# Kernel tuning notes

Hardware: AMD Instinct MI355X
Metric: run time of the kernel (lower is better)

Reference implementation:

```python
import jax, jax.numpy as jnp
import numpy as np

B, T, C, H, HD = 2, 2048, 2048, 16, 128
RD = HD // 2          # rope_dim = 64 (32 complex pairs)
KVR, QR = 512, 1024   # kv_lora_rank, q_lora_rank


def setup_inputs() -> dict:
    key = jax.random.key(0)
    ks = jax.random.split(key, 10)
    s = 0.02
    x = jax.random.normal(ks[0], (B, T, C), jnp.float32)
    w_dq  = jax.random.normal(ks[1], (C, QR),     jnp.float32) * s
    w_uq  = jax.random.normal(ks[2], (QR, H * HD), jnp.float32) * s
    w_dkv = jax.random.normal(ks[3], (C, KVR),    jnp.float32) * s
    w_uk  = jax.random.normal(ks[4], (KVR, H * HD), jnp.float32) * s
    w_uv  = jax.random.normal(ks[5], (KVR, H * HD), jnp.float32) * s
    w_qr  = jax.random.normal(ks[6], (QR, H * RD), jnp.float32) * s
    w_kr  = jax.random.normal(ks[7], (C, H * RD), jnp.float32) * s
    w_o   = jax.random.normal(ks[8], (H * HD, C), jnp.float32) * s
    # rotary frequencies for the rope_dim part (rope_dim//2 = 32 complex freqs)
    inv_freq = 1.0 / (10000.0 ** (jnp.arange(0, RD, 2, dtype=jnp.float32) / RD))
    ang = jnp.arange(T, dtype=jnp.float32)[:, None] * inv_freq[None, :]  # (T, 32)
    return {"x": x, "w_dq": w_dq, "w_uq": w_uq, "w_dkv": w_dkv, "w_uk": w_uk,
            "w_uv": w_uv, "w_qr": w_qr, "w_kr": w_kr, "w_o": w_o,
            "freqs_cos": jnp.cos(ang), "freqs_sin": jnp.sin(ang)}


def _apply_rope(t, cos, sin):
    # t: (B, T, H, rd); cos/sin: (T, rd//2). Complex rotation on adjacent pairs.
    tr, ti = t[..., 0::2], t[..., 1::2]
    c = cos[None, :, None, :]
    s = sin[None, :, None, :]
    out_r = tr * c - ti * s
    out_i = tr * s + ti * c
    return jnp.stack([out_r, out_i], axis=-1).reshape(t.shape)


def reference(x, w_dq, w_uq, w_dkv, w_uk, w_uv, w_qr, w_kr, w_o, freqs_cos, freqs_sin):
    b, t, _ = x.shape
    # low-rank KV path
    c_kv = x @ w_dkv                                   # (B,T,KVR)
    k_c = (c_kv @ w_uk).reshape(b, t, H, HD)
    v   = (c_kv @ w_uv).reshape(b, t, H, HD)
    # low-rank Q path
    c_q = x @ w_dq                                     # (B,T,QR)
    q_c = (c_q @ w_uq).reshape(b, t, H, HD)
    # decoupled rope parts
    q_r = (c_q @ w_qr).reshape(b, t, H, RD)
    k_r = (x @ w_kr).reshape(b, t, H, RD)
    q_r = _apply_rope(q_r, freqs_cos, freqs_sin)
    k_r = _apply_rope(k_r, freqs_cos, freqs_sin)
    # concat content + rope -> head dim D = HD + RD
    q = jnp.concatenate([q_c, q_r], axis=-1).transpose(0, 2, 1, 3)  # (B,H,T,D)
    k = jnp.concatenate([k_c, k_r], axis=-1).transpose(0, 2, 1, 3)
    v = v.transpose(0, 2, 1, 3)                                     # (B,H,T,HD)
    d = q.shape[-1]
    scores = jnp.einsum('bhqd,bhkd->bhqk', q, k) / jnp.sqrt(jnp.float32(d))
    causal = jnp.tril(jnp.ones((t, t), dtype=bool))
    scores = jnp.where(causal[None, None], scores, jnp.float32(-1e30))
    att = jax.nn.softmax(scores, axis=-1)
    out = jnp.einsum('bhqk,bhkd->bhqd', att, v)        # (B,H,T,HD)
    out = out.transpose(0, 2, 1, 3).reshape(b, t, H * HD)
    return out @ w_o
```

## Files before the change

kernel.cpp:

```cpp
#include <hip/hip_runtime.h>

typedef unsigned short ushort_t;
typedef __attribute__((ext_vector_type(8))) short bs8;
typedef __attribute__((ext_vector_type(4))) float f32x4;
typedef __attribute__((ext_vector_type(4))) unsigned short u16x4;

#define DEV __device__ __forceinline__

DEV unsigned short f2bf(float f){
  unsigned u = __float_as_uint(f);
  u += 0x7fffu + ((u >> 16) & 1u);
  return (unsigned short)(u >> 16);
}
DEV float bf2f(unsigned short h){ return __uint_as_float(((unsigned)h) << 16); }

DEV unsigned cvt_pk_bf16(float lo, float hi){
  unsigned r;
  asm volatile("v_cvt_pk_bf16_f32 %0, %1, %2" : "=v"(r) : "v"(lo), "v"(hi));
  return r;
}

DEV void gl2lds16(const void* g, void* l){
  __builtin_amdgcn_global_load_lds((const __attribute__((address_space(1))) void*)g,
                                   (__attribute__((address_space(3))) void*)l, 16, 0, 0);
}

DEV void st_out(ushort_t* C, size_t i, float v){ C[i] = f2bf(v); }
DEV void st_out(float*    C, size_t i, float v){ C[i] = v; }

__global__ __launch_bounds__(256) void cast_x(const float* __restrict__ in,
                                              ushort_t* __restrict__ outb){
  size_t i = ((size_t)blockIdx.x * 256 + threadIdx.x) * 4;
  float4 v = *(const float4*)(in + i);
  u16x4 o;
  o[0] = f2bf(v.x); o[1] = f2bf(v.y); o[2] = f2bf(v.z); o[3] = f2bf(v.w);
  *(u16x4*)(outb + i) = o;
}

__global__ __launch_bounds__(256) void transpose_cast(const float* __restrict__ in,
                                                      ushort_t* __restrict__ out,
                                                      int K, int N){
  __shared__ float tile[32][33];
  int k0 = blockIdx.y * 32, n0 = blockIdx.x * 32;
  int tx = threadIdx.x, ty = threadIdx.y;
  for (int r = ty; r < 32; r += 8)
    tile[r][tx] = in[(size_t)(k0 + r) * N + n0 + tx];
  __syncthreads();
  for (int r = ty; r < 32; r += 8)
    out[(size_t)(n0 + r) * K + k0 + tx] = f2bf(tile[tx][r]);
}

__global__ __launch_bounds__(256) void transpose_v(const ushort_t* __restrict__ v, int ldv,
                                                   ushort_t* __restrict__ vT){
  __shared__ ushort_t tile[32][33];
  int bh = blockIdx.z; int b = bh >> 4, h = bh & 15;
  int t0 = blockIdx.x * 32, d0 = blockIdx.y * 32;
  int tx = threadIdx.x, ty = threadIdx.y;
  for (int r = ty; r < 32; r += 8)
    tile[r][tx] = v[((size_t)(b * 2048 + t0 + r)) * ldv + h * 128 + d0 + tx];
  __syncthreads();
  for (int r = ty; r < 32; r += 8)
    vT[((size_t)bh * 128 + d0 + r) * 2048 + t0 + tx] = tile[tx][r];
}

template<int EPI, typename OT>
__global__ __launch_bounds__(512, 2) void gemm256(const ushort_t* __restrict__ A, int lda,
                                                  const ushort_t* __restrict__ BT,
                                                  OT* __restrict__ C,
                                                  int M, int N, int K,
                                                  ushort_t* __restrict__ aux,
                                                  const float* __restrict__ fcp,
                                                  const float* __restrict__ fsp){
  __shared__ __align__(16) ushort_t lds[65536];
  const int tid = threadIdx.x, lane = tid & 63, wid = tid >> 6;
  const int l15 = lane & 15, lhi = lane >> 4;
  const int wr = wid >> 2, wc = wid & 3;

  const int nbx = M >> 8;
  const int nwg = gridDim.x;
  const int orig = blockIdx.x;
  const int wg = (orig & 7) * (nwg >> 3) + (orig >> 3);
  const int m0 = (wg % nbx) << 8;
  const int n0 = (wg / nbx) << 8;

  const int trow = tid >> 3;
  const int tcsrc = (tid & 7) ^ (trow & 7);
  const ushort_t* gA[2][2];
  const ushort_t* gB[2][2];
#pragma unroll
  for (int h = 0; h < 2; ++h)
#pragma unroll
    for (int i = 0; i < 2; ++i){
      gA[h][i] = A  + (size_t)(m0 + h * 128 + i * 64 + trow) * lda + tcsrc * 8;
      gB[h][i] = BT + (size_t)(n0 + h * 128 + i * 64 + trow) * K   + tcsrc * 8;
    }

  auto STAGE_A = [&](int buf, int h, int kt){
    gl2lds16(gA[h][0] + (size_t)kt * 64, lds + buf * 32768 + h * 8192 + tid * 8);
    gl2lds16(gA[h][1] + (size_t)kt * 64, lds + buf * 32768 + h * 8192 + 4096 + tid * 8);
  };
  auto STAGE_B = [&](int buf, int h, int kt){
    gl2lds16(gB[h][0] + (size_t)kt * 64, lds + buf * 32768 + 16384 + h * 8192 + tid * 8);
    gl2lds16(gB[h][1] + (size_t)kt * 64, lds + buf * 32768 + 16384 + h * 8192 + 4096 + tid * 8);
  };

  const int ck0 = ((lhi) ^ (l15 & 7)) << 3;
  const int ck1 = ((4 + lhi) ^ (l15 & 7)) << 3;

  f32x4 acc[8][4] = {};
  bs8 aF[4][2], bLo[2][2], bHi[2][2];

  auto RDA = [&](int buf, int mq){
#pragma unroll
    for (int m = 0; m < 4; ++m){
      const ushort_t* r = lds + buf * 32768 + wr * 8192 + ((mq + m) * 16 + l15) * 64;
      aF[m][0] = *(const bs8*)(r + ck0);
      aF[m][1] = *(const bs8*)(r + ck1);
    }
  };
  auto RDB = [&](int buf, int nq, bs8 (&br)[2][2]){
#pragma unroll
    for (int n = 0; n < 2; ++n){
      const ushort_t* r = lds + buf * 32768 + 16384 + (wc >> 1) * 8192 +
                          ((wc & 1) * 64 + (nq + n) * 16 + l15) * 64;
      br[n][0] = *(const bs8*)(r + ck0);
      br[n][1] = *(const bs8*)(r + ck1);
    }
  };
  auto MMA = [&](int mq, int nq, bs8 (&br)[2][2]){
    __builtin_amdgcn_s_setprio(1);
#pragma unroll
    for (int m = 0; m < 4; ++m)
#pragma unroll
      for (int n = 0; n < 2; ++n){
        acc[mq + m][nq + n] = __builtin_amdgcn_mfma_f32_16x16x32_bf16(aF[m][0], br[n][0], acc[mq + m][nq + n], 0, 0, 0);
        acc[mq + m][nq + n] = __builtin_amdgcn_mfma_f32_16x16x32_bf16(aF[m][1], br[n][1], acc[mq + m][nq + n], 0, 0, 0);
      }
    __builtin_amdgcn_s_setprio(0);
  };

#define BAR() __builtin_amdgcn_s_barrier()
#define LGK() asm volatile("s_waitcnt lgkmcnt(0)" ::: "memory")
#define VMC4() asm volatile("s_waitcnt vmcnt(4)" ::: "memory")

  const int nkt = K >> 6;
  const int nIter = K >> 7;

  STAGE_A(0, 0, 0); STAGE_A(0, 1, 0); STAGE_B(0, 0, 0); STAGE_B(0, 1, 0);
  STAGE_B(1, 0, 1); STAGE_B(1, 1, 1);
  VMC4();
  BAR();

  for (int it = 0; it < nIter; ++it){
    const int kt1 = 2 * it + 1;
    int kt2 = 2 * it + 2; if (kt2 > nkt - 1) kt2 = nkt - 1;
    int kt3 = 2 * it + 3; if (kt3 > nkt - 1) kt3 = nkt - 1;
    RDA(0, 0); RDB(0, 0, bLo);
    STAGE_A(1, 0, kt1);
    BAR(); LGK(); MMA(0, 0, bLo); BAR();
    RDB(0, 2, bHi);
    STAGE_A(1, 1, kt1);
    BAR(); LGK(); MMA(0, 2, bHi); BAR();
    RDA(0, 4);
    STAGE_B(0, 0, kt2);
    BAR(); LGK(); MMA(4, 0, bLo); BAR();
    STAGE_B(0, 1, kt2);
    BAR(); LGK(); MMA(4, 2, bHi);
    VMC4(); BAR();
    RDA(1, 0); RDB(1, 0, bLo);
    STAGE_A(0, 0, kt2);
    BAR(); LGK(); MMA(0, 0, bLo); BAR();
    RDB(1, 2, bHi);
    STAGE_A(0, 1, kt2);
    BAR(); LGK(); MMA(0, 2, bHi); BAR();
    RDA(1, 4);
    STAGE_B(1, 0, kt3);
    BAR(); LGK(); MMA(4, 0, bLo); BAR();
    STAGE_B(1, 1, kt3);
    BAR(); LGK(); MMA(4, 2, bHi);
    VMC4(); BAR();
  }
#undef BAR
#undef LGK
#undef VMC4

  const float SC = (EPI == 2) ? (0.07216878364870323f * 1.4426950408889634f) : 1.0f;
  const int RBASE = (EPI == 1) ? 1536 : 2048;
#pragma unroll
  for (int m = 0; m < 8; ++m){
    const int r = m0 + wr * 128 + m * 16 + lhi * 4;
#pragma unroll
    for (int n = 0; n < 4; ++n){
      const int c = n0 + wc * 64 + n * 16 + l15;
      if (EPI == 0){
#pragma unroll
        for (int j = 0; j < 4; ++j)
          st_out(C, (size_t)(r + j) * N + c, acc[m][n][j]);
      } else if ((EPI == 1 && c < 1536)){
#pragma unroll
        for (int j = 0; j < 4; ++j)
          C[(size_t)(r + j) * 1536 + c] = (OT)f2bf(acc[m][n][j]);
      } else if (EPI == 2 && c < 2048){
        int hh = c >> 7, d = c & 127;
#pragma unroll
        for (int j = 0; j < 4; ++j){
          int rr = r + j, bb = rr >> 11, tt = rr & 2047;
          aux[((size_t)(bb * 16 + hh) * 2048 + tt) * 192 + d] = f2bf(acc[m][n][j] * SC);
        }
      } else if (EPI == 3 && c < 2048){
        int hh = c >> 7, d = c & 127;
#pragma unroll
        for (int j = 0; j < 4; ++j){
          int rr = r + j, bb = rr >> 11, tt = rr & 2047;
          aux[((size_t)(bb * 16 + hh) * 2048 + tt) * 192 + d] = f2bf(acc[m][n][j]);
        }
      } else if (EPI == 3){
#pragma unroll
        for (int j = 0; j < 4; ++j)
          C[(size_t)(r + j) * 2048 + (c - 2048)] = (OT)f2bf(acc[m][n][j]);
      } else {
        int cr = c - RBASE;
        int hh = cr >> 6, dr = cr & 63, ii = dr >> 1;
#pragma unroll
        for (int j = 0; j < 4; ++j){
          int rr = r + j, bb = rr >> 11, tt = rr & 2047;
          float v = acc[m][n][j] * SC;
          float pv = __shfl_xor(v, 1);
          float co = fcp[tt * 32 + ii], si = fsp[tt * 32 + ii];
          float o = (l15 & 1) ? fmaf(pv, si, v * co) : fmaf(-pv, si, v * co);
          aux[((size_t)(bb * 16 + hh) * 2048 + tt) * 192 + 128 + dr] = f2bf(o);
        }
      }
    }
  }
}

__global__ __launch_bounds__(512, 1) void attn_kernel(const ushort_t* __restrict__ Qa,
                                                      const ushort_t* __restrict__ Ka,
                                                      const ushort_t* __restrict__ VT,
                                                      ushort_t* __restrict__ O){
  __shared__ __align__(16) ushort_t lds[40960];
  const int tid = threadIdx.x, lane = tid & 63, wid = tid >> 6;
  const int bh = blockIdx.x, p = blockIdx.y;
  const int b = bh >> 4, h = bh & 15;
  const int qb0 = 15 - p, qb1 = p;
  const int nkt0 = 2 * qb0 + 2;
  const int NT = 34;
  const int l15 = lane & 15, lhi = lane >> 4;

  const ushort_t* Kbh = Ka + (size_t)bh * 2048 * 192;
  const ushort_t* Vbh = VT + (size_t)bh * 128 * 2048;

  const ushort_t* ksrc[3];
#pragma unroll
  for (int i = 0; i < 3; ++i){
    int c = i * 512 + tid;
    int row = c / 24, col = c % 24;
    int hk = (row & 3) | (((row >> 3) & 1) << 2);
    ksrc[i] = Kbh + (size_t)row * 192 + (col ^ hk) * 8;
  }
  const ushort_t* vsrc[2];
#pragma unroll
  for (int i = 0; i < 2; ++i){
    int c = i * 512 + tid;
    int d = c >> 3, col = c & 7;
    vsrc[i] = Vbh + (size_t)d * 2048 + (col ^ (d & 7)) * 8;
  }

  auto STAGE = [&](int ft, int buf){
    int kt = (ft < nkt0) ? ft : ft - nkt0;
#pragma unroll
    for (int i = 0; i < 3; ++i)
      gl2lds16(ksrc[i] + (size_t)kt * 12288, lds + buf * 12288 + (i * 512 + tid) * 8);
#pragma unroll
    for (int i = 0; i < 2; ++i)
      gl2lds16(vsrc[i] + kt * 64, lds + 24576 + buf * 8192 + (i * 512 + tid) * 8);
  };

  bs8 qf[6];
  auto LOADQ = [&](int qb){
    const size_t qrow = ((size_t)bh * 2048 + qb * 128 + wid * 16 + l15) * 192;
#pragma unroll
    for (int kc = 0; kc < 6; ++kc)
      qf[kc] = *(const bs8*)(Qa + qrow + kc * 32 + lhi * 8);
  };

  f32x4 acc[8] = {};
  float mrow = -1e30f, lrow = 0.f;

  auto EPI = [&](int qb){
    float rl = 1.0f / lrow;
    int t = qb * 128 + wid * 16 + l15;
#pragma unroll
    for (int f = 0; f < 8; ++f){
      u16x4 o;
#pragma unroll
      for (int j = 0; j < 4; ++j) o[j] = f2bf(acc[f][j] * rl);
      *(u16x4*)(O + ((size_t)b * 2048 + t) * 2048 + h * 128 + f * 16 + lhi * 4) = o;
    }
  };

  const int hkr = (l15 & 3) | (((l15 >> 2) & 1) << 2);

#define BARR() __builtin_amdgcn_s_barrier()
#define LGK0() asm volatile("s_waitcnt lgkmcnt(0)" ::: "memory")
#define VMC(n) asm volatile("s_waitcnt vmcnt(" #n ")" ::: "memory")

  LOADQ(qb0);
  STAGE(0, 0);
  STAGE(1, 1);
  VMC(5);
  BARR();

  for (int ft = 0; ft < NT; ++ft){
    if (ft == nkt0){
      EPI(qb0);
#pragma unroll
      for (int f = 0; f < 8; ++f) acc[f] = (f32x4){0.f, 0.f, 0.f, 0.f};
      mrow = -1e30f; lrow = 0.f;
      LOADQ(qb1);
    }
    const int seg = (ft >= nkt0) ? 1 : 0;
    const int kt = seg ? ft - nkt0 : ft;
    const int qb = seg ? qb1 : qb0;
    const int qm0 = qb << 7;
    const int mylast = 2 * qb + (wid >> 2);
    const int cur = ft & 1;
    const ushort_t* Kb = lds + cur * 12288;
    const ushort_t* Vb = lds + 24576 + cur * 8192;

    if (kt <= mylast){
      f32x4 s[4] = {};
      __builtin_amdgcn_s_setprio(1);
#pragma unroll
      for (int kc = 0; kc < 6; ++kc){
        bs8 kf4[4];
#pragma unroll
        for (int m = 0; m < 4; ++m){
          int row = ((m >> 1) << 5) + ((l15 >> 2) << 3) + ((m & 1) << 2) + (l15 & 3);
          kf4[m] = *(const bs8*)(Kb + row * 192 + (((kc * 4 + lhi) ^ hkr) << 3));
        }
#pragma unroll
        for (int m = 0; m < 4; ++m)
          s[m] = __builtin_amdgcn_mfma_f32_16x16x32_bf16(kf4[m], qf[kc], s[m], 0, 0, 0);
      }
      __builtin_amdgcn_s_setprio(0);

      const bool noMask = (kt * 64 + 63) <= (qm0 + wid * 16);
      const int qi = qm0 + wid * 16 + l15;
      float rmax = -3e38f;
#pragma unroll
      for (int m = 0; m < 4; ++m)
#pragma unroll
        for (int j = 0; j < 4; ++j){
          float sv = s[m][j];
          if (!noMask){
            int ki = kt * 64 + ((m >> 1) << 5) + (lhi << 3) + ((m & 1) << 2) + j;
            if (ki > qi) sv = -3e38f;
          }
          s[m][j] = sv;
          rmax = fmaxf(rmax, sv);
        }
      rmax = fmaxf(rmax, __shfl_xor(rmax, 16));
      rmax = fmaxf(rmax, __shfl_xor(rmax, 32));
      if (!__all(rmax <= mrow + 8.f)){
        float mnew = fmaxf(mrow, rmax);
        float osc = exp2f(mrow - mnew);
        lrow *= osc;
#pragma unroll
        for (int f = 0; f < 8; ++f) acc[f] *= osc;
        mrow = mnew;
      }
      float rsum = 0.f;
#pragma unroll
      for (int m = 0; m < 4; ++m)
#pragma unroll
        for (int j = 0; j < 4; ++j){
          float pv = exp2f(s[m][j] - mrow);
          s[m][j] = pv;
          rsum += pv;
        }
      rsum += __shfl_xor(rsum, 16);
      rsum += __shfl_xor(rsum, 32);
      lrow += rsum;

      bs8 pb[2];
#pragma unroll
      for (int kc2 = 0; kc2 < 2; ++kc2){
        union { bs8 v; unsigned u[4]; } pu;
#pragma unroll
        for (int half = 0; half < 2; ++half){
          const f32x4& sv = s[2 * kc2 + half];
          pu.u[2 * half]     = cvt_pk_bf16(sv[0], sv[1]);
          pu.u[2 * half + 1] = cvt_pk_bf16(sv[2], sv[3]);
        }
        pb[kc2] = pu.v;
      }

      __builtin_amdgcn_s_setprio(1);
#pragma unroll
      for (int kc2 = 0; kc2 < 2; ++kc2)
#pragma unroll
        for (int f = 0; f < 8; ++f){
          bs8 vf = *(const bs8*)(Vb + (f * 16 + l15) * 64 + (((kc2 * 4 + lhi) ^ (l15 & 7)) << 3));
          acc[f] = __builtin_amdgcn_mfma_f32_16x16x32_bf16(vf, pb[kc2], acc[f], 0, 0, 0);
        }
      __builtin_amdgcn_s_setprio(0);
    }

    LGK0();
    BARR();
    if (ft + 2 < NT){
      STAGE(ft + 2, cur);
      VMC(5);
    } else {
      VMC(0);
    }
    BARR();
  }
#undef BARR
#undef LGK0
#undef VMC

  EPI(qb1);
}

extern "C" void kernel_launch(void* const* d_in, const int* in_sizes, int n_in,
                              void* d_out, int out_size, void* d_ws, size_t ws_size,
                              hipStream_t stream){
  constexpr int Bc = 2, Tc = 2048, Cc = 2048, Hc = 16, HDc = 128, RDc = 64, KVRc = 512, QRc = 1024;
  constexpr int Mx = Bc * Tc;
  const float* x     = (const float*)d_in[0];
  const float* w_dq  = (const float*)d_in[1];
  const float* w_uq  = (const float*)d_in[2];
  const float* w_dkv = (const float*)d_in[3];
  const float* w_uk  = (const float*)d_in[4];
  const float* w_uv  = (const float*)d_in[5];
  const float* w_qr  = (const float*)d_in[6];
  const float* w_kr  = (const float*)d_in[7];
  const float* w_o   = (const float*)d_in[8];
  const float* fc    = (const float*)d_in[9];
  const float* fs    = (const float*)d_in[10];
  float* out = (float*)d_out;

  char* ws = (char*)d_ws;
  size_t off = 0;
  auto alloc = [&](size_t elems) -> ushort_t* {
    ushort_t* p = (ushort_t*)(ws + off);
    off += ((elems * 2) + 255) & ~(size_t)255;
    return p;
  };
  ushort_t* xb    = alloc((size_t)Mx * Cc);
  ushort_t* wdqT  = alloc((size_t)QRc * Cc);
  ushort_t* wdkvT = alloc((size_t)KVRc * Cc);
  ushort_t* wkrT  = alloc((size_t)(Hc * RDc) * Cc);
  ushort_t* wuqT  = alloc((size_t)(Hc * HDc) * QRc);
  ushort_t* wqrT  = alloc((size_t)(Hc * RDc) * QRc);
  ushort_t* wukT  = alloc((size_t)(Hc * HDc) * KVRc);
  ushort_t* wuvT  = alloc((size_t)(Hc * HDc) * KVRc);
  ushort_t* woT   = alloc((size_t)Cc * (Hc * HDc));
  ushort_t* comb1 = alloc((size_t)Mx * 1536);
  ushort_t* vb    = alloc((size_t)Mx * 2048);
  ushort_t* Qa    = alloc((size_t)Bc * Hc * Tc * 192);
  ushort_t* Ka    = alloc((size_t)Bc * Hc * Tc * 192);
  ushort_t* vT    = alloc((size_t)Bc * Hc * HDc * Tc);
  ushort_t* O     = xb;

  cast_x<<<dim3(((size_t)Mx * Cc) / 1024), 256, 0, stream>>>(x, xb);

  transpose_cast<<<dim3(QRc / 32, Cc / 32), dim3(32, 8), 0, stream>>>(w_dq, wdqT, Cc, QRc);
  transpose_cast<<<dim3(KVRc / 32, Cc / 32), dim3(32, 8), 0, stream>>>(w_dkv, wdkvT, Cc, KVRc);
  transpose_cast<<<dim3((Hc * RDc) / 32, Cc / 32), dim3(32, 8), 0, stream>>>(w_kr, wkrT, Cc, Hc * RDc);
  transpose_cast<<<dim3((Hc * HDc) / 32, QRc / 32), dim3(32, 8), 0, stream>>>(w_uq, wuqT, QRc, Hc * HDc);
  transpose_cast<<<dim3((Hc * RDc) / 32, QRc / 32), dim3(32, 8), 0, stream>>>(w_qr, wqrT, QRc, Hc * RDc);
  transpose_cast<<<dim3((Hc * HDc) / 32, KVRc / 32), dim3(32, 8), 0, stream>>>(w_uk, wukT, KVRc, Hc * HDc);
  transpose_cast<<<dim3((Hc * HDc) / 32, KVRc / 32), dim3(32, 8), 0, stream>>>(w_uv, wuvT, KVRc, Hc * HDc);
  transpose_cast<<<dim3(Cc / 32, (Hc * HDc) / 32), dim3(32, 8), 0, stream>>>(w_o, woT, Hc * HDc, Cc);

  gemm256<1, ushort_t><<<dim3((Mx / 256) * (2560 / 256)), 512, 0, stream>>>(
      xb, Cc, wdqT, comb1, Mx, 2560, Cc, Ka, fc, fs);
  gemm256<2, ushort_t><<<dim3((Mx / 256) * (3072 / 256)), 512, 0, stream>>>(
      comb1, 1536, wuqT, Qa , Mx, 3072, QRc, Qa, fc, fs);
  gemm256<3, ushort_t><<<dim3((Mx / 256) * (4096 / 256)), 512, 0, stream>>>(
      comb1 + QRc, 1536, wukT, vb, Mx, 4096, KVRc, Ka, fc, fs);

  transpose_v<<<dim3(Tc / 32, HDc / 32, Bc * Hc), dim3(32, 8), 0, stream>>>(vb, 2048, vT);

  attn_kernel<<<dim3(Bc * Hc, 8), 512, 0, stream>>>(Qa, Ka, vT, O);

  gemm256<0, float><<<dim3((Mx / 256) * (Cc / 256)), 512, 0, stream>>>(
      O, Hc * HDc, woT, out, Mx, Cc, Hc * HDc, nullptr, nullptr, nullptr);
}
```

Before: 317.3 us.

## Batch weight casts, merge up-projection GEMMs, split attention KV tiles across wave halves

Replaces eight transpose-cast launches with one flat-grid kernel, and fuses the Q and K/V up-projection GEMMs into a single 448-block launch so they share one wave of work. In attention, each wave now handles 32 query rows and the two wave halves process alternating KV tiles, then merge partial softmax states through extra LDS at the epilogue. This aims to cut launch overhead, tail effects and causal load imbalance, at the cost of more LDS, more registers for the attention kernel and an extra merge step.

```diff
diff --git a/kernel.cpp b/kernel.cpp
--- a/kernel.cpp
+++ b/kernel.cpp
@@ -37,17 +37,34 @@
   *(u16x4*)(outb + i) = o;
 }
 
-__global__ __launch_bounds__(256) void transpose_cast(const float* __restrict__ in,
-                                                      ushort_t* __restrict__ out,
-                                                      int K, int N){
+__global__ __launch_bounds__(256) void tcast_all(
+    const float* __restrict__ s0, const float* __restrict__ s1,
+    const float* __restrict__ s2, const float* __restrict__ s3,
+    const float* __restrict__ s4, const float* __restrict__ s5,
+    const float* __restrict__ s6, const float* __restrict__ s7,
+    ushort_t* __restrict__ d0, ushort_t* __restrict__ d1,
+    ushort_t* __restrict__ d2, ushort_t* __restrict__ d3,
+    ushort_t* __restrict__ d4, ushort_t* __restrict__ d5,
+    ushort_t* __restrict__ d6, ushort_t* __restrict__ d7){
   __shared__ float tile[32][33];
-  int k0 = blockIdx.y * 32, n0 = blockIdx.x * 32;
-  int tx = threadIdx.x, ty = threadIdx.y;
+  const int bid = blockIdx.x;
+  const float* src; ushort_t* dst; int K, N, loc;
+  if      (bid <  2048){ src=s0; dst=d0; K=2048; N=1024; loc=bid; }
+  else if (bid <  3072){ src=s1; dst=d1; K=2048; N=512;  loc=bid-2048; }
+  else if (bid <  5120){ src=s2; dst=d2; K=2048; N=1024; loc=bid-3072; }
+  else if (bid <  7168){ src=s3; dst=d3; K=1024; N=2048; loc=bid-5120; }
+  else if (bid <  8192){ src=s4; dst=d4; K=1024; N=1024; loc=bid-7168; }
+  else if (bid <  9216){ src=s5; dst=d5; K=512;  N=2048; loc=bid-8192; }
+  else if (bid < 10240){ src=s6; dst=d6; K=512;  N=2048; loc=bid-9216; }
+  else                 { src=s7; dst=d7; K=2048; N=2048; loc=bid-10240; }
+  const int nx = N >> 5;
+  const int n0 = (loc % nx) << 5, k0 = (loc / nx) << 5;
+  const int tx = threadIdx.x & 31, ty = threadIdx.x >> 5;
   for (int r = ty; r < 32; r += 8)
-    tile[r][tx] = in[(size_t)(k0 + r) * N + n0 + tx];
+    tile[r][tx] = src[(size_t)(k0 + r) * N + n0 + tx];
   __syncthreads();
   for (int r = ty; r < 32; r += 8)
-    out[(size_t)(n0 + r) * K + k0 + tx] = f2bf(tile[tx][r]);
+    dst[(size_t)(n0 + r) * K + k0 + tx] = f2bf(tile[tx][r]);
 }
 
 __global__ __launch_bounds__(256) void transpose_v(const ushort_t* __restrict__ v, int ldv,
@@ -63,25 +80,12 @@
     vT[((size_t)bh * 128 + d0 + r) * 2048 + t0 + tx] = tile[tx][r];
 }
 
-template<int EPI, typename OT>
-__global__ __launch_bounds__(512, 2) void gemm256(const ushort_t* __restrict__ A, int lda,
-                                                  const ushort_t* __restrict__ BT,
-                                                  OT* __restrict__ C,
-                                                  int M, int N, int K,
-                                                  ushort_t* __restrict__ aux,
-                                                  const float* __restrict__ fcp,
-                                                  const float* __restrict__ fsp){
-  __shared__ __align__(16) ushort_t lds[65536];
+DEV void gemm_core(const ushort_t* __restrict__ A, int lda,
+                   const ushort_t* __restrict__ BT, int K,
+                   int m0, int n0, ushort_t* lds, f32x4 (&acc)[8][4]){
   const int tid = threadIdx.x, lane = tid & 63, wid = tid >> 6;
   const int l15 = lane & 15, lhi = lane >> 4;
   const int wr = wid >> 2, wc = wid & 3;
-
-  const int nbx = M >> 8;
-  const int nwg = gridDim.x;
-  const int orig = blockIdx.x;
-  const int wg = (orig & 7) * (nwg >> 3) + (orig >> 3);
-  const int m0 = (wg % nbx) << 8;
-  const int n0 = (wg / nbx) << 8;
 
   const int trow = tid >> 3;
   const int tcsrc = (tid & 7) ^ (trow & 7);
@@ -107,7 +111,6 @@
   const int ck0 = ((lhi) ^ (l15 & 7)) << 3;
   const int ck1 = ((4 + lhi) ^ (l15 & 7)) << 3;
 
-  f32x4 acc[8][4] = {};
   bs8 aF[4][2], bLo[2][2], bHi[2][2];
 
   auto RDA = [&](int buf, int mq){
@@ -183,7 +186,15 @@
 #undef BAR
 #undef LGK
 #undef VMC4
-
+}
+
+template<int EPI, typename OT>
+DEV void gemm_epi(f32x4 (&acc)[8][4], OT* __restrict__ C, int N, int m0, int n0,
+                  ushort_t* __restrict__ aux,
+                  const float* __restrict__ fcp, const float* __restrict__ fsp){
+  const int tid = threadIdx.x, lane = tid & 63, wid = tid >> 6;
+  const int l15 = lane & 15, lhi = lane >> 4;
+  const int wr = wid >> 2, wc = wid & 3;
   const float SC = (EPI == 2) ? (0.07216878364870323f * 1.4426950408889634f) : 1.0f;
   const int RBASE = (EPI == 1) ? 1536 : 2048;
 #pragma unroll
@@ -235,12 +246,60 @@
   }
 }
 
+template<int EPI, typename OT>
+__global__ __launch_bounds__(512, 2) void gemm256(const ushort_t* __restrict__ A, int lda,
+                                                  const ushort_t* __restrict__ BT,
+                                                  OT* __restrict__ C,
+                                                  int M, int N, int K,
+                                                  ushort_t* __restrict__ aux,
+                                                  const float* __restrict__ fcp,
+                                                  const float* __restrict__ fsp){
+  __shared__ __align__(16) ushort_t lds[65536];
+  const int nbx = M >> 8;
+  const int nwg = gridDim.x;
+  const int orig = blockIdx.x;
+  const int wg = (orig & 7) * (nwg >> 3) + (orig >> 3);
+  const int m0 = (wg % nbx) << 8;
+  const int n0 = (wg / nbx) << 8;
+  f32x4 acc[8][4] = {};
+  gemm_core(A, lda, BT, K, m0, n0, lds, acc);
+  gemm_epi<EPI, OT>(acc, C, N, m0, n0, aux, fcp, fsp);
+}
+
+__global__ __launch_bounds__(512, 2) void gemm23(const ushort_t* __restrict__ A2,
+                                                 const ushort_t* __restrict__ BT2,
+                                                 const ushort_t* __restrict__ A3,
+                                                 const ushort_t* __restrict__ BT3,
+                                                 ushort_t* __restrict__ vb,
+                                                 ushort_t* __restrict__ Qa,
+                                                 ushort_t* __restrict__ Ka,
+                                                 const float* __restrict__ fcp,
+                                                 const float* __restrict__ fsp){
+  __shared__ __align__(16) ushort_t lds[65536];
+  const int nwg = gridDim.x;
+  const int orig = blockIdx.x;
+  const int wg = (orig & 7) * (nwg >> 3) + (orig >> 3);
+  f32x4 acc[8][4] = {};
+  if (wg < 192){
+    const int m0 = (wg % 16) << 8, n0 = (wg / 16) << 8;
+    gemm_core(A2, 1536, BT2, 1024, m0, n0, lds, acc);
+    gemm_epi<2, ushort_t>(acc, nullptr, 3072, m0, n0, Qa, fcp, fsp);
+  } else {
+    const int g = wg - 192;
+    const int m0 = (g % 16) << 8, n0 = (g / 16) << 8;
+    gemm_core(A3, 1536, BT3, 512, m0, n0, lds, acc);
+    gemm_epi<3, ushort_t>(acc, vb, 4096, m0, n0, Ka, fcp, fsp);
+  }
+}
+
 __global__ __launch_bounds__(512, 1) void attn_kernel(const ushort_t* __restrict__ Qa,
                                                       const ushort_t* __restrict__ Ka,
                                                       const ushort_t* __restrict__ VT,
                                                       ushort_t* __restrict__ O){
-  __shared__ __align__(16) ushort_t lds[40960];
+  __shared__ __align__(16) ushort_t lds[40960 + 34816];
+  float* fm = (float*)(lds + 40960);
   const int tid = threadIdx.x, lane = tid & 63, wid = tid >> 6;
+  const int sw = wid & 3, par = wid >> 2;
   const int bh = blockIdx.x, p = blockIdx.y;
   const int b = bh >> 4, h = bh & 15;
   const int qb0 = 15 - p, qb1 = p;
@@ -277,26 +336,52 @@
       gl2lds16(vsrc[i] + kt * 64, lds + 24576 + buf * 8192 + (i * 512 + tid) * 8);
   };
 
-  bs8 qf[6];
+  bs8 qf[2][6];
   auto LOADQ = [&](int qb){
-    const size_t qrow = ((size_t)bh * 2048 + qb * 128 + wid * 16 + l15) * 192;
-#pragma unroll
-    for (int kc = 0; kc < 6; ++kc)
-      qf[kc] = *(const bs8*)(Qa + qrow + kc * 32 + lhi * 8);
-  };
-
-  f32x4 acc[8] = {};
-  float mrow = -1e30f, lrow = 0.f;
-
-  auto EPI = [&](int qb){
-    float rl = 1.0f / lrow;
-    int t = qb * 128 + wid * 16 + l15;
-#pragma unroll
-    for (int f = 0; f < 8; ++f){
-      u16x4 o;
-#pragma unroll
-      for (int j = 0; j < 4; ++j) o[j] = f2bf(acc[f][j] * rl);
-      *(u16x4*)(O + ((size_t)b * 2048 + t) * 2048 + h * 128 + f * 16 + lhi * 4) = o;
+#pragma unroll
+    for (int qg = 0; qg < 2; ++qg){
+      const size_t qrow = ((size_t)bh * 2048 + qb * 128 + sw * 32 + qg * 16 + l15) * 192;
+#pragma unroll
+      for (int kc = 0; kc < 6; ++kc)
+        qf[qg][kc] = *(const bs8*)(Qa + qrow + kc * 32 + lhi * 8);
+    }
+  };
+
+  f32x4 acc[2][8] = {};
+  float mrow[2] = {-1e30f, -1e30f};
+  float lrow[2] = {0.f, 0.f};
+
+  auto MERGE_EPI = [&](int qb){
+    if (par == 1){
+#pragma unroll
+      for (int qg = 0; qg < 2; ++qg)
+#pragma unroll
+        for (int f = 0; f < 8; ++f)
+          *(f32x4*)(fm + sw * 4096 + (qg * 8 + f) * 256 + lane * 4) = acc[qg][f];
+      f32x4 ml;
+      ml[0] = mrow[0]; ml[1] = lrow[0]; ml[2] = mrow[1]; ml[3] = lrow[1];
+      *(f32x4*)(fm + 16384 + sw * 256 + lane * 4) = ml;
+    }
+    __syncthreads();
+    if (par == 0){
+      f32x4 ml = *(const f32x4*)(fm + 16384 + sw * 256 + lane * 4);
+#pragma unroll
+      for (int qg = 0; qg < 2; ++qg){
+        float m1 = ml[2 * qg], l1 = ml[2 * qg + 1];
+        float mm = fmaxf(mrow[qg], m1);
+        float f0 = exp2f(mrow[qg] - mm), f1v = exp2f(m1 - mm);
+        float rl = 1.0f / (lrow[qg] * f0 + l1 * f1v);
+        int t = qb * 128 + sw * 32 + qg * 16 + l15;
+#pragma unroll
+        for (int f = 0; f < 8; ++f){
+          f32x4 a1 = *(const f32x4*)(fm + sw * 4096 + (qg * 8 + f) * 256 + lane * 4);
+          u16x4 o;
+#pragma unroll
+          for (int j = 0; j < 4; ++j)
+            o[j] = f2bf((acc[qg][f][j] * f0 + a1[j] * f1v) * rl);
+          *(u16x4*)(O + ((size_t)b * 2048 + t) * 2048 + h * 128 + f * 16 + lhi * 4) = o;
+        }
+      }
     }
   };
 
@@ -314,23 +399,25 @@
 
   for (int ft = 0; ft < NT; ++ft){
     if (ft == nkt0){
-      EPI(qb0);
-#pragma unroll
-      for (int f = 0; f < 8; ++f) acc[f] = (f32x4){0.f, 0.f, 0.f, 0.f};
-      mrow = -1e30f; lrow = 0.f;
+      MERGE_EPI(qb0);
+#pragma unroll
+      for (int qg = 0; qg < 2; ++qg)
+#pragma unroll
+        for (int f = 0; f < 8; ++f) acc[qg][f] = (f32x4){0.f, 0.f, 0.f, 0.f};
+      mrow[0] = mrow[1] = -1e30f; lrow[0] = lrow[1] = 0.f;
       LOADQ(qb1);
     }
     const int seg = (ft >= nkt0) ? 1 : 0;
     const int kt = seg ? ft - nkt0 : ft;
     const int qb = seg ? qb1 : qb0;
     const int qm0 = qb << 7;
-    const int mylast = 2 * qb + (wid >> 2);
+    const int mylast = 2 * qb + (sw >> 1);
     const int cur = ft & 1;
     const ushort_t* Kb = lds + cur * 12288;
     const ushort_t* Vb = lds + 24576 + cur * 8192;
 
-    if (kt <= mylast){
-      f32x4 s[4] = {};
+    if (((kt & 1) == par) && kt <= mylast){
+      f32x4 s[2][4] = {};
       __builtin_amdgcn_s_setprio(1);
 #pragma unroll
       for (int kc = 0; kc < 6; ++kc){
@@ -341,60 +428,65 @@
           kf4[m] = *(const bs8*)(Kb + row * 192 + (((kc * 4 + lhi) ^ hkr) << 3));
         }
 #pragma unroll
-        for (int m = 0; m < 4; ++m)
-          s[m] = __builtin_amdgcn_mfma_f32_16x16x32_bf16(kf4[m], qf[kc], s[m], 0, 0, 0);
+        for (int qg = 0; qg < 2; ++qg)
+#pragma unroll
+          for (int m = 0; m < 4; ++m)
+            s[qg][m] = __builtin_amdgcn_mfma_f32_16x16x32_bf16(kf4[m], qf[qg][kc], s[qg][m], 0, 0, 0);
       }
       __builtin_amdgcn_s_setprio(0);
 
-      const bool noMask = (kt * 64 + 63) <= (qm0 + wid * 16);
-      const int qi = qm0 + wid * 16 + l15;
-      float rmax = -3e38f;
-#pragma unroll
-      for (int m = 0; m < 4; ++m)
-#pragma unroll
-        for (int j = 0; j < 4; ++j){
-          float sv = s[m][j];
-          if (!noMask){
-            int ki = kt * 64 + ((m >> 1) << 5) + (lhi << 3) + ((m & 1) << 2) + j;
-            if (ki > qi) sv = -3e38f;
+      const bool noMask = (kt * 64 + 63) <= (qm0 + sw * 32);
+      bs8 pb[2][2];
+#pragma unroll
+      for (int qg = 0; qg < 2; ++qg){
+        const int qi = qm0 + sw * 32 + qg * 16 + l15;
+        float rmax = -3e38f;
+#pragma unroll
+        for (int m = 0; m < 4; ++m)
+#pragma unroll
+          for (int j = 0; j < 4; ++j){
+            float sv = s[qg][m][j];
+            if (!noMask){
+              int ki = kt * 64 + ((m >> 1) << 5) + (lhi << 3) + ((m & 1) << 2) + j;
+              if (ki > qi) sv = -3e38f;
+            }
+            s[qg][m][j] = sv;
+            rmax = fmaxf(rmax, sv);
           }
-          s[m][j] = sv;
-          rmax = fmaxf(rmax, sv);
-        }
-      rmax = fmaxf(rmax, __shfl_xor(rmax, 16));
-      rmax = fmaxf(rmax, __shfl_xor(rmax, 32));
-      if (!__all(rmax <= mrow + 8.f)){
-        float mnew = fmaxf(mrow, rmax);
-        float osc = exp2f(mrow - mnew);
-        lrow *= osc;
-#pragma unroll
-        for (int f = 0; f < 8; ++f) acc[f] *= osc;
-        mrow = mnew;
-      }
-      float rsum = 0.f;
-#pragma unroll
-      for (int m = 0; m < 4; ++m)
-#pragma unroll
-        for (int j = 0; j < 4; ++j){
-          float pv = exp2f(s[m][j] - mrow);
-          s[m][j] = pv;
-          rsum += pv;
-        }
-      rsum += __shfl_xor(rsum, 16);
-      rsum += __shfl_xor(rsum, 32);
-      lrow += rsum;
-
-      bs8 pb[2];
-#pragma unroll
-      for (int kc2 = 0; kc2 < 2; ++kc2){
-        union { bs8 v; unsigned u[4]; } pu;
-#pragma unroll
-        for (int half = 0; half < 2; ++half){
-          const f32x4& sv = s[2 * kc2 + half];
-          pu.u[2 * half]     = cvt_pk_bf16(sv[0], sv[1]);
-          pu.u[2 * half + 1] = cvt_pk_bf16(sv[2], sv[3]);
-        }
-        pb[kc2] = pu.v;
+        rmax = fmaxf(rmax, __shfl_xor(rmax, 16));
+        rmax = fmaxf(rmax, __shfl_xor(rmax, 32));
+        if (!__all(rmax <= mrow[qg] + 8.f)){
+          float mnew = fmaxf(mrow[qg], rmax);
+          float osc = exp2f(mrow[qg] - mnew);
+          lrow[qg] *= osc;
+#pragma unroll
+          for (int f = 0; f < 8; ++f) acc[qg][f] *= osc;
+          mrow[qg] = mnew;
+        }
+        float rsum = 0.f;
+#pragma unroll
+        for (int m = 0; m < 4; ++m)
+#pragma unroll
+          for (int j = 0; j < 4; ++j){
+            float pv = exp2f(s[qg][m][j] - mrow[qg]);
+            s[qg][m][j] = pv;
+            rsum += pv;
+          }
+        rsum += __shfl_xor(rsum, 16);
+        rsum += __shfl_xor(rsum, 32);
+        lrow[qg] += rsum;
+
+#pragma unroll
+        for (int kc2 = 0; kc2 < 2; ++kc2){
+          union { bs8 v; unsigned u[4]; } pu;
+#pragma unroll
+          for (int half = 0; half < 2; ++half){
+            const f32x4& sv = s[qg][2 * kc2 + half];
+            pu.u[2 * half]     = cvt_pk_bf16(sv[0], sv[1]);
+            pu.u[2 * half + 1] = cvt_pk_bf16(sv[2], sv[3]);
+          }
+          pb[qg][kc2] = pu.v;
+        }
       }
 
       __builtin_amdgcn_s_setprio(1);
@@ -403,7 +495,9 @@
 #pragma unroll
         for (int f = 0; f < 8; ++f){
           bs8 vf = *(const bs8*)(Vb + (f * 16 + l15) * 64 + (((kc2 * 4 + lhi) ^ (l15 & 7)) << 3));
-          acc[f] = __builtin_amdgcn_mfma_f32_16x16x32_bf16(vf, pb[kc2], acc[f], 0, 0, 0);
+#pragma unroll
+          for (int qg = 0; qg < 2; ++qg)
+            acc[qg][f] = __builtin_amdgcn_mfma_f32_16x16x32_bf16(vf, pb[qg][kc2], acc[qg][f], 0, 0, 0);
         }
       __builtin_amdgcn_s_setprio(0);
     }
@@ -422,7 +516,7 @@
 #undef LGK0
 #undef VMC
 
-  EPI(qb1);
+  MERGE_EPI(qb1);
 }
 
 extern "C" void kernel_launch(void* const* d_in, const int* in_sizes, int n_in,
@@ -468,21 +562,12 @@
 
   cast_x<<<dim3(((size_t)Mx * Cc) / 1024), 256, 0, stream>>>(x, xb);
 
-  transpose_cast<<<dim3(QRc / 32, Cc / 32), dim3(32, 8), 0, stream>>>(w_dq, wdqT, Cc, QRc);
-  transpose_cast<<<dim3(KVRc / 32, Cc / 32), dim3(32, 8), 0, stream>>>(w_dkv, wdkvT, Cc, KVRc);
-  transpose_cast<<<dim3((Hc * RDc) / 32, Cc / 32), dim3(32, 8), 0, stream>>>(w_kr, wkrT, Cc, Hc * RDc);
-  transpose_cast<<<dim3((Hc * HDc) / 32, QRc / 32), dim3(32, 8), 0, stream>>>(w_uq, wuqT, QRc, Hc * HDc);
-  transpose_cast<<<dim3((Hc * RDc) / 32, QRc / 32), dim3(32, 8), 0, stream>>>(w_qr, wqrT, QRc, Hc * RDc);
-  transpose_cast<<<dim3((Hc * HDc) / 32, KVRc / 32), dim3(32, 8), 0, stream>>>(w_uk, wukT, KVRc, Hc * HDc);
-  transpose_cast<<<dim3((Hc * HDc) / 32, KVRc / 32), dim3(32, 8), 0, stream>>>(w_uv, wuvT, KVRc, Hc * HDc);
-  transpose_cast<<<dim3(Cc / 32, (Hc * HDc) / 32), dim3(32, 8), 0, stream>>>(w_o, woT, Hc * HDc, Cc);
+  tcast_all<<<dim3(14336), 256, 0, stream>>>(w_dq, w_dkv, w_kr, w_uq, w_qr, w_uk, w_uv, w_o,
+                                             wdqT, wdkvT, wkrT, wuqT, wqrT, wukT, wuvT, woT);
 
   gemm256<1, ushort_t><<<dim3((Mx / 256) * (2560 / 256)), 512, 0, stream>>>(
       xb, Cc, wdqT, comb1, Mx, 2560, Cc, Ka, fc, fs);
-  gemm256<2, ushort_t><<<dim3((Mx / 256) * (3072 / 256)), 512, 0, stream>>>(
-      comb1, 1536, wuqT, Qa , Mx, 3072, QRc, Qa, fc, fs);
-  gemm256<3, ushort_t><<<dim3((Mx / 256) * (4096 / 256)), 512, 0, stream>>>(
-      comb1 + QRc, 1536, wukT, vb, Mx, 4096, KVRc, Ka, fc, fs);
+  gemm23<<<dim3(448), 512, 0, stream>>>(comb1, wuqT, comb1 + QRc, wukT, vb, Qa, Ka, fc, fs);
 
   transpose_v<<<dim3(Tc / 32, HDc / 32, Bc * Hc), dim3(32, 8), 0, stream>>>(vb, 2048, vT);
 
```

Result: slower. 333.9 us (+5.2%).
